# Kernel optimization log

Hardware: AMD Instinct MI355X
Metric: run time of the kernel (lower is better)

## Reference

```python
import jax, jax.numpy as jnp
import numpy as np

B, T, C = 4, 2048, 1024
H, D = 16, 64  # num_heads, head_dim
WINDOW = 256


def setup_inputs() -> dict:
    key = jax.random.key(0)
    k_x, k_qkv, k_proj, k_qb, k_pb = jax.random.split(key, 5)
    x = jax.random.normal(k_x, (B, T, C), dtype=jnp.float32)
    # xavier-uniform-ish init for qkv weight (as in _reset_parameters)
    lim_qkv = float(np.sqrt(6.0 / (C + 3 * C)))
    qkv_w = jax.random.uniform(k_qkv, (3 * C, C), minval=-lim_qkv, maxval=lim_qkv, dtype=jnp.float32)
    qkv_b = jax.random.normal(k_qb, (3 * C,), dtype=jnp.float32) * 0.02
    lim_p = float(np.sqrt(1.0 / C))
    proj_w = jax.random.uniform(k_proj, (C, C), minval=-lim_p, maxval=lim_p, dtype=jnp.float32)
    proj_b = jax.random.normal(k_pb, (C,), dtype=jnp.float32) * 0.02
    # windowed causal mask: attend to j iff j <= i and i - j < WINDOW
    i = jnp.arange(T)[:, None]
    j = jnp.arange(T)[None, :]
    attn_mask = (j <= i) & (i - j < WINDOW)  # [T, T] bool
    return {"x": x, "attn_mask": attn_mask, "qkv_w": qkv_w, "qkv_b": qkv_b,
            "proj_w": proj_w, "proj_b": proj_b}


def reference(x, attn_mask, qkv_w, qkv_b, proj_w, proj_b):
    qkv = (x @ qkv_w.T + qkv_b).reshape(B, T, 3, H, D)
    qkv = jnp.transpose(qkv, (2, 0, 3, 1, 4))
    q, k, v = qkv[0], qkv[1], qkv[2]
    scale = 1.0 / jnp.sqrt(jnp.asarray(D, dtype=q.dtype))
    scores = jnp.einsum('bhqd,bhkd->bhqk', q, k) * scale  # [B,H,T,T]
    neg = jnp.asarray(jnp.finfo(scores.dtype).min, dtype=scores.dtype)
    scores = jnp.where(attn_mask[None, None], scores, neg)
    attn = jax.nn.softmax(scores, axis=-1)
    out = jnp.einsum('bhqk,bhkd->bhqd', attn, v)  # [B,H,T,D]
    out = jnp.transpose(out, (0, 2, 1, 3)).reshape(B, T, C)
    out = out @ proj_w.T + proj_b
    return out
```

## Files before the change

### kernel.cpp

```cpp
#include <hip/hip_runtime.h>

#define BB 4
#define TT 2048
#define CC 1024
#define HH 16
#define DD 64
#define WIN 256

typedef __attribute__((ext_vector_type(8))) short short8;
typedef __attribute__((ext_vector_type(4))) float floatx4;
typedef unsigned short u16;

typedef __attribute__((address_space(3))) void lds_void;
typedef const __attribute__((address_space(1))) void g_void;

__device__ __forceinline__ void gl_lds16(const u16* g, u16* l) {
    __builtin_amdgcn_global_load_lds((g_void*)g, (lds_void*)l, 16, 0, 0);
}

__device__ __forceinline__ float bf2f(u16 u) {
    union { unsigned int i; float f; } v; v.i = ((unsigned int)u) << 16; return v.f;
}
__device__ __forceinline__ u16 f2bf(float f) {
    union { float f; unsigned int i; } v; v.f = f;
    unsigned int x = v.i;
    x += ((x >> 16) & 1u) + 0x7FFFu;
    return (u16)(x >> 16);
}

__global__ void cvt_all(const float* __restrict__ x, const float* __restrict__ qw,
                        const float* __restrict__ pw,
                        u16* __restrict__ xb, u16* __restrict__ wb, u16* __restrict__ pwb) {
    int bid = blockIdx.x;
    const float* src; u16* dst; int off;
    if (bid < 4096)      { src = x;  dst = xb;  off = bid; }
    else if (bid < 5632) { src = qw; dst = wb;  off = bid - 4096; }
    else                 { src = pw; dst = pwb; off = bid - 5632; }
    int i = (off * 256 + (int)threadIdx.x) * 8;
    float4 a = *(const float4*)(src + i);
    float4 b = *(const float4*)(src + i + 4);
    u16 o[8] = { f2bf(a.x), f2bf(a.y), f2bf(a.z), f2bf(a.w),
                 f2bf(b.x), f2bf(b.y), f2bf(b.z), f2bf(b.w) };
    *(uint4*)(dst + i) = *(const uint4*)o;
}


__global__ __launch_bounds__(256) void gemm_qkv(
    const u16* __restrict__ A, const u16* __restrict__ Bw,
    const float* __restrict__ bias,
    u16* __restrict__ Qb, u16* __restrict__ Kb, u16* __restrict__ Vb)
{
    const int K = CC;
    __shared__ u16 As[4096];
    __shared__ u16 Bs[4096];
    const int tid = threadIdx.x;
    const int wave = tid >> 6, lane = tid & 63;
    const int wm = wave >> 1, wn = wave & 1;
    const int quad = lane >> 4, l15 = lane & 15;
    const int bN = blockIdx.x * 128, bM = blockIdx.y * 128;

    const int srow0 = wave * 16 + (lane >> 2);
    const int srow1 = (wave + 4) * 16 + (lane >> 2);
    const int schunk = ((lane & 3) ^ ((lane >> 3) & 3)) * 8;
    const u16* gA0 = A + (size_t)(bM + srow0) * K + schunk;
    const u16* gA1 = A + (size_t)(bM + srow1) * K + schunk;
    const u16* gB0 = Bw + (size_t)(bN + srow0) * K + schunk;
    const u16* gB1 = Bw + (size_t)(bN + srow1) * K + schunk;
    u16* lA0 = &As[wave * 512];
    u16* lA1 = &As[(wave + 4) * 512];
    u16* lB0 = &Bs[wave * 512];
    u16* lB1 = &Bs[(wave + 4) * 512];

    const int rdoff = l15 * 32 + ((quad ^ ((l15 >> 1) & 3)) * 8);

    floatx4 acc[4][4] = {};

    for (int k0 = 0; k0 < K; k0 += 32) {
        __syncthreads();
        gl_lds16(gA0 + k0, lA0);
        gl_lds16(gA1 + k0, lA1);
        gl_lds16(gB0 + k0, lB0);
        gl_lds16(gB1 + k0, lB1);
        __syncthreads();
        short8 af[4], bf[4];
#pragma unroll
        for (int i = 0; i < 4; ++i) {
            af[i] = *(const short8*)&As[(wm * 4 + i) * 512 + rdoff];
            bf[i] = *(const short8*)&Bs[(wn * 4 + i) * 512 + rdoff];
        }
#pragma unroll
        for (int mi = 0; mi < 4; ++mi)
#pragma unroll
            for (int ni = 0; ni < 4; ++ni)
                acc[mi][ni] = __builtin_amdgcn_mfma_f32_16x16x32_bf16(af[mi], bf[ni], acc[mi][ni], 0, 0, 0);
    }

#pragma unroll
    for (int mi = 0; mi < 4; ++mi)
#pragma unroll
        for (int ni = 0; ni < 4; ++ni) {
            int col = bN + wn * 64 + ni * 16 + l15;
            float bv = bias[col];
            int which = col >> 10, rem = col & 1023;
            int h = rem >> 6, d = rem & 63;
            u16* dst = which == 0 ? Qb : (which == 1 ? Kb : Vb);
#pragma unroll
            for (int rg = 0; rg < 4; ++rg) {
                int row = bM + wm * 64 + mi * 16 + quad * 4 + rg;
                int b = row >> 11, t = row & 2047;
                float v = acc[mi][ni][rg] + bv;
                dst[(((size_t)(b * HH + h)) * TT + t) * DD + d] = f2bf(v);
            }
        }
}

__global__ __launch_bounds__(256) void gemm_proj(
    const u16* __restrict__ A, const u16* __restrict__ Bw,
    const float* __restrict__ bias, float* __restrict__ Out)
{
    const int K = CC;
    __shared__ u16 As[4096];
    __shared__ u16 Bs[4096];
    const int tid = threadIdx.x;
    const int wave = tid >> 6, lane = tid & 63;
    const int wm = wave >> 1, wn = wave & 1;
    const int quad = lane >> 4, l15 = lane & 15;
    const int bN = blockIdx.x * 128, bM = blockIdx.y * 128;

    const int srow0 = wave * 16 + (lane >> 2);
    const int srow1 = (wave + 4) * 16 + (lane >> 2);
    const int schunk = ((lane & 3) ^ ((lane >> 3) & 3)) * 8;
    const u16* gA0 = A + (size_t)(bM + srow0) * K + schunk;
    const u16* gA1 = A + (size_t)(bM + srow1) * K + schunk;
    const u16* gB0 = Bw + (size_t)(bN + srow0) * K + schunk;
    const u16* gB1 = Bw + (size_t)(bN + srow1) * K + schunk;
    u16* lA0 = &As[wave * 512];
    u16* lA1 = &As[(wave + 4) * 512];
    u16* lB0 = &Bs[wave * 512];
    u16* lB1 = &Bs[(wave + 4) * 512];

    const int rdoff = l15 * 32 + ((quad ^ ((l15 >> 1) & 3)) * 8);

    floatx4 acc[4][4] = {};

    for (int k0 = 0; k0 < K; k0 += 32) {
        __syncthreads();
        gl_lds16(gA0 + k0, lA0);
        gl_lds16(gA1 + k0, lA1);
        gl_lds16(gB0 + k0, lB0);
        gl_lds16(gB1 + k0, lB1);
        __syncthreads();
        short8 af[4], bf[4];
#pragma unroll
        for (int i = 0; i < 4; ++i) {
            af[i] = *(const short8*)&As[(wm * 4 + i) * 512 + rdoff];
            bf[i] = *(const short8*)&Bs[(wn * 4 + i) * 512 + rdoff];
        }
#pragma unroll
        for (int mi = 0; mi < 4; ++mi)
#pragma unroll
            for (int ni = 0; ni < 4; ++ni)
                acc[mi][ni] = __builtin_amdgcn_mfma_f32_16x16x32_bf16(af[mi], bf[ni], acc[mi][ni], 0, 0, 0);
    }

#pragma unroll
    for (int mi = 0; mi < 4; ++mi)
#pragma unroll
        for (int ni = 0; ni < 4; ++ni) {
            int col = bN + wn * 64 + ni * 16 + l15;
            float bv = bias[col];
#pragma unroll
            for (int rg = 0; rg < 4; ++rg) {
                int row = bM + wm * 64 + mi * 16 + quad * 4 + rg;
                Out[(size_t)row * CC + col] = acc[mi][ni][rg] + bv;
            }
        }
}

__global__ __launch_bounds__(256) void attn_mfma(
    const u16* __restrict__ Qb, const u16* __restrict__ Kb, const u16* __restrict__ Vb,
    u16* __restrict__ Y)
{
    __shared__ u16 Ks[64][72];
    __shared__ u16 Vt[64][72];
    __shared__ u16 Ps[4][16][72];

    const int tid = threadIdx.x;
    const int wave = tid >> 6, lane = tid & 63;
    const int quad = lane >> 4, l15 = lane & 15;
    const int q0 = blockIdx.x * 64;
    const int bh = blockIdx.y;
    const int b = bh >> 4, h = bh & 15;
    const u16* Qp = Qb + (size_t)bh * TT * DD;
    const u16* Kp = Kb + (size_t)bh * TT * DD;
    const u16* Vp = Vb + (size_t)bh * TT * DD;
    const int qw = q0 + wave * 16;

    short8 qf[2];
    qf[0] = *(const short8*)&Qp[(size_t)(qw + l15) * DD + quad * 8];
    qf[1] = *(const short8*)&Qp[(size_t)(qw + l15) * DD + 32 + quad * 8];

    float m_i[4] = { -1e30f, -1e30f, -1e30f, -1e30f };
    float l_i[4] = { 0.f, 0.f, 0.f, 0.f };
    floatx4 Oacc[4] = {};

    const int kb = (q0 >= WIN) ? (q0 - WIN) : 0;
    for (int j0 = kb; j0 < q0 + 64; j0 += 64) {
        __syncthreads();
#pragma unroll
        for (int it = 0; it < 2; ++it) {
            int slot = tid + it * 256;
            int j = slot >> 3, c8 = (slot & 7) << 3;
            *(uint4*)&Ks[j][c8] = *(const uint4*)&Kp[(size_t)(j0 + j) * DD + c8];
        }
#pragma unroll
        for (int it = 0; it < 2; ++it) {
            int slot = tid + it * 256;
            int j = slot >> 3, d0 = (slot & 7) << 3;
            uint4 raw = *(const uint4*)&Vp[(size_t)(j0 + j) * DD + d0];
            const u16* u = (const u16*)&raw;
#pragma unroll
            for (int i = 0; i < 8; ++i) {
                int d = d0 + i;
                int col = (((j >> 3) ^ (d >> 3)) << 3) + (j & 7);
                Vt[d][col] = u[i];
            }
        }
        __syncthreads();

        floatx4 Sacc[4] = {};
#pragma unroll
        for (int nt = 0; nt < 4; ++nt) {
            short8 kf0 = *(const short8*)&Ks[nt * 16 + l15][quad * 8];
            short8 kf1 = *(const short8*)&Ks[nt * 16 + l15][32 + quad * 8];
            Sacc[nt] = __builtin_amdgcn_mfma_f32_16x16x32_bf16(qf[0], kf0, Sacc[nt], 0, 0, 0);
            Sacc[nt] = __builtin_amdgcn_mfma_f32_16x16x32_bf16(qf[1], kf1, Sacc[nt], 0, 0, 0);
        }

        float mc[4] = { -1e30f, -1e30f, -1e30f, -1e30f };
#pragma unroll
        for (int nt = 0; nt < 4; ++nt)
#pragma unroll
            for (int r = 0; r < 4; ++r) {
                int q = qw + quad * 4 + r;
                int j = j0 + nt * 16 + l15;
                float s = (j <= q && (q - j) < WIN) ? Sacc[nt][r] * 0.125f : -1e30f;
                Sacc[nt][r] = s;
                mc[r] = fmaxf(mc[r], s);
            }
#pragma unroll
        for (int m = 1; m < 16; m <<= 1)
#pragma unroll
            for (int r = 0; r < 4; ++r) mc[r] = fmaxf(mc[r], __shfl_xor(mc[r], m, 64));

        float alpha[4];
#pragma unroll
        for (int r = 0; r < 4; ++r) {
            float mn = fmaxf(m_i[r], mc[r]);
            alpha[r] = __expf(m_i[r] - mn);
            m_i[r] = mn;
        }
        float rs[4] = { 0.f, 0.f, 0.f, 0.f };
#pragma unroll
        for (int nt = 0; nt < 4; ++nt)
#pragma unroll
            for (int r = 0; r < 4; ++r) {
                float s = Sacc[nt][r];
                float p = (s > -1e29f) ? __expf(s - m_i[r]) : 0.f;
                Sacc[nt][r] = p;
                rs[r] += p;
            }
#pragma unroll
        for (int m = 1; m < 16; m <<= 1)
#pragma unroll
            for (int r = 0; r < 4; ++r) rs[r] += __shfl_xor(rs[r], m, 64);
#pragma unroll
        for (int r = 0; r < 4; ++r) l_i[r] = l_i[r] * alpha[r] + rs[r];
#pragma unroll
        for (int dt = 0; dt < 4; ++dt)
#pragma unroll
            for (int r = 0; r < 4; ++r) Oacc[dt][r] *= alpha[r];

#pragma unroll
        for (int nt = 0; nt < 4; ++nt)
#pragma unroll
            for (int r = 0; r < 4; ++r)
                Ps[wave][quad * 4 + r][nt * 16 + l15] = f2bf(Sacc[nt][r]);

#pragma unroll
        for (int ks = 0; ks < 2; ++ks) {
            short8 pf = *(const short8*)&Ps[wave][l15][ks * 32 + quad * 8];
#pragma unroll
            for (int dt = 0; dt < 4; ++dt) {
                int d = dt * 16 + l15;
                int col = (((ks * 4 + quad) ^ (d >> 3)) << 3);
                short8 vf = *(const short8*)&Vt[d][col];
                Oacc[dt] = __builtin_amdgcn_mfma_f32_16x16x32_bf16(pf, vf, Oacc[dt], 0, 0, 0);
            }
        }
    }

    float inv[4];
#pragma unroll
    for (int r = 0; r < 4; ++r) inv[r] = 1.f / l_i[r];
#pragma unroll
    for (int dt = 0; dt < 4; ++dt)
#pragma unroll
        for (int r = 0; r < 4; ++r) {
            int t = qw + quad * 4 + r;
            int d = dt * 16 + l15;
            Y[((size_t)b * TT + t) * CC + h * DD + d] = f2bf(Oacc[dt][r] * inv[r]);
        }
}

extern "C" void kernel_launch(void* const* d_in, const int* in_sizes, int n_in,
                              void* d_out, int out_size, void* d_ws, size_t ws_size,
                              hipStream_t stream) {
    const float* x      = (const float*)d_in[0];
    const float* qkv_w  = (const float*)d_in[2];
    const float* qkv_b  = (const float*)d_in[3];
    const float* proj_w = (const float*)d_in[4];
    const float* proj_b = (const float*)d_in[5];
    float* out = (float*)d_out;

    u16* xb  = (u16*)d_ws;
    u16* wb  = xb  + (size_t)8192 * 1024;
    u16* pwb = wb  + (size_t)3072 * 1024;
    u16* Qb  = pwb + (size_t)1024 * 1024;
    u16* Kb  = Qb  + (size_t)64 * 2048 * 64;
    u16* Vb  = Kb  + (size_t)64 * 2048 * 64;
    u16* Yb  = Vb  + (size_t)64 * 2048 * 64;

    cvt_all<<<6144, 256, 0, stream>>>(x, qkv_w, proj_w, xb, wb, pwb);
    gemm_qkv<<<dim3(24, 64), 256, 0, stream>>>(xb, wb, qkv_b, Qb, Kb, Vb);
    attn_mfma<<<dim3(TT / 64, BB * HH), 256, 0, stream>>>(Qb, Kb, Vb, Yb);
    gemm_proj<<<dim3(8, 64), 256, 0, stream>>>(Yb, pwb, proj_b, out);
}
```

Measured before the change: 238.5 us.

## Pipeline QKV GEMM with 256x256 tiles, 8 waves and double-buffered LDS

Rewrites the QKV projection GEMM to use 256x256 block tiles with 512 threads, a double-buffered LDS staging scheme of 64-wide K slices, and interleaved direct-to-LDS global loads with MFMA phases gated by partial vmcnt waits and s_barrier. MFMA sections are raised in priority with s_setprio. The intent is to hide global-load latency behind compute and raise arithmetic intensity per block. In exchange it uses 128KB of LDS per block and more accumulators per wave, which limits occupancy, and the schedule depends on getting the barrier and waitcnt placement right.

After: 245.0 us. 1.03x slower.

```diff
diff --git a/kernel.cpp b/kernel.cpp
--- a/kernel.cpp
+++ b/kernel.cpp
@@ -44,71 +44,109 @@
     *(uint4*)(dst + i) = *(const uint4*)o;
 }
 
-
-__global__ __launch_bounds__(256) void gemm_qkv(
+#define NT_QKV 16
+
+__global__ __launch_bounds__(512, 2) void gemm_qkv(
     const u16* __restrict__ A, const u16* __restrict__ Bw,
     const float* __restrict__ bias,
     u16* __restrict__ Qb, u16* __restrict__ Kb, u16* __restrict__ Vb)
 {
     const int K = CC;
-    __shared__ u16 As[4096];
-    __shared__ u16 Bs[4096];
+    __shared__ u16 lds[2][4][8192];
+
     const int tid = threadIdx.x;
     const int wave = tid >> 6, lane = tid & 63;
-    const int wm = wave >> 1, wn = wave & 1;
+    const int wm = wave >> 2, wn = wave & 3;
     const int quad = lane >> 4, l15 = lane & 15;
-    const int bN = blockIdx.x * 128, bM = blockIdx.y * 128;
-
-    const int srow0 = wave * 16 + (lane >> 2);
-    const int srow1 = (wave + 4) * 16 + (lane >> 2);
-    const int schunk = ((lane & 3) ^ ((lane >> 3) & 3)) * 8;
-    const u16* gA0 = A + (size_t)(bM + srow0) * K + schunk;
-    const u16* gA1 = A + (size_t)(bM + srow1) * K + schunk;
-    const u16* gB0 = Bw + (size_t)(bN + srow0) * K + schunk;
-    const u16* gB1 = Bw + (size_t)(bN + srow1) * K + schunk;
-    u16* lA0 = &As[wave * 512];
-    u16* lA1 = &As[(wave + 4) * 512];
-    u16* lB0 = &Bs[wave * 512];
-    u16* lB1 = &Bs[(wave + 4) * 512];
+    const int bN = blockIdx.x * 256, bM = blockIdx.y * 256;
+
+    const int n0 = tid, n1 = tid + 512;
+    const int r0 = (n0 >> 6) * 16 + ((n0 & 63) >> 2);
+    const int r1 = (n1 >> 6) * 16 + ((n1 & 63) >> 2);
+    const int c0 = (n0 & 3) ^ ((r0 >> 1) & 3);
+    const int c1 = (n1 & 3) ^ ((r1 >> 1) & 3);
+    const u16* gA0 = A + (size_t)(bM + r0) * K + c0 * 8;
+    const u16* gA1 = A + (size_t)(bM + r1) * K + c1 * 8;
+    const u16* gB0 = Bw + (size_t)(bN + r0) * K + c0 * 8;
+    const u16* gB1 = Bw + (size_t)(bN + r1) * K + c1 * 8;
 
     const int rdoff = l15 * 32 + ((quad ^ ((l15 >> 1) & 3)) * 8);
 
-    floatx4 acc[4][4] = {};
-
-    for (int k0 = 0; k0 < K; k0 += 32) {
-        __syncthreads();
-        gl_lds16(gA0 + k0, lA0);
-        gl_lds16(gA1 + k0, lA1);
-        gl_lds16(gB0 + k0, lB0);
-        gl_lds16(gB1 + k0, lB1);
-        __syncthreads();
+    floatx4 acc[8][4] = {};
+
+#define STG_A(buf, kh, t) do { const int ko = (t) * 64 + (kh) * 32;          \
+        gl_lds16(gA0 + ko, &lds[buf][kh][wave * 512]);                       \
+        gl_lds16(gA1 + ko, &lds[buf][kh][4096 + wave * 512]); } while (0)
+#define STG_B(buf, kh, t) do { const int ko = (t) * 64 + (kh) * 32;          \
+        gl_lds16(gB0 + ko, &lds[buf][2 + (kh)][wave * 512]);                 \
+        gl_lds16(gB1 + ko, &lds[buf][2 + (kh)][4096 + wave * 512]); } while (0)
+#define LDA(buf, kk, qm) do { _Pragma("unroll")                              \
+        for (int i = 0; i < 4; ++i)                                          \
+            af[i] = *(const short8*)&lds[buf][kk][(wm * 8 + (qm) * 4 + i) * 512 + rdoff]; } while (0)
+#define LDB(buf, kk) do { _Pragma("unroll")                                  \
+        for (int j = 0; j < 4; ++j)                                          \
+            bf[j] = *(const short8*)&lds[buf][2 + (kk)][(wn * 4 + j) * 512 + rdoff]; } while (0)
+#define MM(qm) do { __builtin_amdgcn_s_setprio(1); _Pragma("unroll")         \
+        for (int i = 0; i < 4; ++i) { _Pragma("unroll")                      \
+            for (int j = 0; j < 4; ++j)                                      \
+                acc[(qm) * 4 + i][j] = __builtin_amdgcn_mfma_f32_16x16x32_bf16( \
+                    af[i], bf[j], acc[(qm) * 4 + i][j], 0, 0, 0); }          \
+        __builtin_amdgcn_s_setprio(0); } while (0)
+#define BARX() do { asm volatile("" ::: "memory");                           \
+        __builtin_amdgcn_s_barrier();                                        \
+        asm volatile("" ::: "memory"); } while (0)
+#define VM6() asm volatile("s_waitcnt vmcnt(6)" ::: "memory")
+
+    STG_B(0, 0, 0); STG_A(0, 0, 0); STG_B(0, 1, 0); STG_A(0, 1, 0);
+    STG_B(1, 0, 1); STG_A(1, 0, 1); STG_B(1, 1, 1);
+    VM6();
+    BARX();
+
+    for (int ii = 0; ii < NT_QKV / 2; ++ii) {
+        const int t0 = 2 * ii, t1 = 2 * ii + 1;
+        const int t2 = (t0 + 2 < NT_QKV) ? t0 + 2 : t0;
+        const int t3 = (t1 + 2 < NT_QKV) ? t1 + 2 : t1;
         short8 af[4], bf[4];
-#pragma unroll
-        for (int i = 0; i < 4; ++i) {
-            af[i] = *(const short8*)&As[(wm * 4 + i) * 512 + rdoff];
-            bf[i] = *(const short8*)&Bs[(wn * 4 + i) * 512 + rdoff];
-        }
-#pragma unroll
-        for (int mi = 0; mi < 4; ++mi)
-#pragma unroll
-            for (int ni = 0; ni < 4; ++ni)
-                acc[mi][ni] = __builtin_amdgcn_mfma_f32_16x16x32_bf16(af[mi], bf[ni], acc[mi][ni], 0, 0, 0);
+        LDA(0, 0, 0); LDB(0, 0); STG_A(1, 1, t1);
+        BARX(); MM(0); BARX();
+        LDA(0, 0, 1); STG_B(0, 0, t2);
+        BARX(); MM(1); BARX();
+        LDA(0, 1, 0); LDB(0, 1); STG_A(0, 0, t2);
+        BARX(); MM(0); BARX();
+        LDA(0, 1, 1); STG_B(0, 1, t2); VM6();
+        BARX(); MM(1); BARX();
+        LDA(1, 0, 0); LDB(1, 0); STG_A(0, 1, t2);
+        BARX(); MM(0); BARX();
+        LDA(1, 0, 1); STG_B(1, 0, t3);
+        BARX(); MM(1); BARX();
+        LDA(1, 1, 0); LDB(1, 1); STG_A(1, 0, t3);
+        BARX(); MM(0); BARX();
+        LDA(1, 1, 1); STG_B(1, 1, t3); VM6();
+        BARX(); MM(1); BARX();
     }
 
-#pragma unroll
-    for (int mi = 0; mi < 4; ++mi)
-#pragma unroll
-        for (int ni = 0; ni < 4; ++ni) {
-            int col = bN + wn * 64 + ni * 16 + l15;
+#undef STG_A
+#undef STG_B
+#undef LDA
+#undef LDB
+#undef MM
+#undef BARX
+#undef VM6
+
+#pragma unroll
+    for (int mf = 0; mf < 8; ++mf)
+#pragma unroll
+        for (int nf = 0; nf < 4; ++nf) {
+            int col = bN + wn * 64 + nf * 16 + l15;
             float bv = bias[col];
             int which = col >> 10, rem = col & 1023;
             int h = rem >> 6, d = rem & 63;
             u16* dst = which == 0 ? Qb : (which == 1 ? Kb : Vb);
 #pragma unroll
             for (int rg = 0; rg < 4; ++rg) {
-                int row = bM + wm * 64 + mi * 16 + quad * 4 + rg;
+                int row = bM + wm * 128 + mf * 16 + quad * 4 + rg;
                 int b = row >> 11, t = row & 2047;
-                float v = acc[mi][ni][rg] + bv;
+                float v = acc[mf][nf][rg] + bv;
                 dst[(((size_t)(b * HH + h)) * TT + t) * DD + d] = f2bf(v);
             }
         }
@@ -332,7 +370,7 @@
     u16* Yb  = Vb  + (size_t)64 * 2048 * 64;
 
     cvt_all<<<6144, 256, 0, stream>>>(x, qkv_w, proj_w, xb, wb, pwb);
-    gemm_qkv<<<dim3(24, 64), 256, 0, stream>>>(xb, wb, qkv_b, Qb, Kb, Vb);
+    gemm_qkv<<<dim3(12, 32), 512, 0, stream>>>(xb, wb, qkv_b, Qb, Kb, Vb);
     attn_mfma<<<dim3(TT / 64, BB * HH), 256, 0, stream>>>(Qb, Kb, Vb, Yb);
     gemm_proj<<<dim3(8, 64), 256, 0, stream>>>(Yb, pwb, proj_b, out);
 }
```

## Pipeline both GEMMs with double-buffered async LDS staging and larger tiles

Applied to the files above, without the earlier changes.

Rewrites the shared QKV and projection GEMM body to use 512-thread blocks with 256x128 output tiles. Global-to-LDS loads are double-buffered at 64-wide K steps, and partial vmcnt waits let the next K slice load while MFMAs run. Block IDs are swizzled so neighbouring blocks reuse the same tiles in L2, and s_setprio raises priority around the MFMA bursts. The larger LDS footprint (about 96KB per block) limits residency to one block per CU, and the last iterations issue redundant clamped loads.

After: 263.2 us. 10.4% more time.

```diff
diff --git a/kernel.cpp b/kernel.cpp
--- a/kernel.cpp
+++ b/kernel.cpp
@@ -45,137 +45,118 @@
 }
 
 
-__global__ __launch_bounds__(256) void gemm_qkv(
-    const u16* __restrict__ A, const u16* __restrict__ Bw,
+#define STG(buf, kh, t) do { const int ko = (t) * 64 + (kh) * 32;            \
+        gl_lds16(gA0 + ko, &lA[buf][kh][wave * 512]);                        \
+        gl_lds16(gA1 + ko, &lA[buf][kh][4096 + wave * 512]);                 \
+        gl_lds16(gB0 + ko, &lB[buf][kh][wave * 512]); } while (0)
+#define LDAB(buf, kk) do { _Pragma("unroll")                                 \
+        for (int i = 0; i < 4; ++i)                                          \
+            af[i] = *(const short8*)&lA[buf][kk][(wm * 4 + i) * 512 + rdoff];\
+        _Pragma("unroll")                                                    \
+        for (int j = 0; j < 4; ++j)                                          \
+            bf[j] = *(const short8*)&lB[buf][kk][(wn * 4 + j) * 512 + rdoff]; } while (0)
+#define MM() do { __builtin_amdgcn_s_setprio(1); _Pragma("unroll")           \
+        for (int i = 0; i < 4; ++i) { _Pragma("unroll")                      \
+            for (int j = 0; j < 4; ++j)                                      \
+                acc[i][j] = __builtin_amdgcn_mfma_f32_16x16x32_bf16(         \
+                    af[i], bf[j], acc[i][j], 0, 0, 0); }                     \
+        __builtin_amdgcn_s_setprio(0); } while (0)
+#define BARX() do { asm volatile("" ::: "memory");                           \
+        __builtin_amdgcn_s_barrier();                                        \
+        asm volatile("" ::: "memory"); } while (0)
+#define VM6() asm volatile("s_waitcnt vmcnt(6)" ::: "memory")
+
+#define GEMM_BODY                                                            \
+    const int K = CC;                                                        \
+    __shared__ u16 lA[2][2][8192];                                           \
+    __shared__ u16 lB[2][2][4096];                                           \
+    const int tid = threadIdx.x;                                             \
+    const int wave = tid >> 6, lane = tid & 63;                              \
+    const int wm = wave >> 1, wn = wave & 1;                                 \
+    const int quad = lane >> 4, l15 = lane & 15;                             \
+    const int r0 = wave * 16 + (lane >> 2);                                  \
+    const int r1 = r0 + 128;                                                 \
+    const int c0 = (lane & 3) ^ ((r0 >> 1) & 3);                             \
+    const u16* gA0 = Amat + (size_t)(bM + r0) * K + c0 * 8;                  \
+    const u16* gA1 = Amat + (size_t)(bM + r1) * K + c0 * 8;                  \
+    const u16* gB0 = Bw + (size_t)(bN + r0) * K + c0 * 8;                    \
+    const int rdoff = l15 * 32 + ((quad ^ ((l15 >> 1) & 3)) * 8);            \
+    floatx4 acc[4][4] = {};                                                  \
+    STG(0, 0, 0); STG(0, 1, 0); STG(1, 0, 1);                                \
+    VM6(); BARX();                                                           \
+    for (int ii = 0; ii < 8; ++ii) {                                         \
+        const int t0 = 2 * ii, t1 = t0 + 1;                                  \
+        const int t2 = (t0 + 2 < 16) ? t0 + 2 : t0;                          \
+        const int t3 = (t1 + 2 < 16) ? t1 + 2 : t1;                          \
+        short8 af[4], bf[4];                                                 \
+        LDAB(0, 0); STG(1, 1, t1); VM6(); BARX(); MM(); BARX();              \
+        LDAB(0, 1); STG(0, 0, t2); VM6(); BARX(); MM(); BARX();              \
+        LDAB(1, 0); STG(0, 1, t2); VM6(); BARX(); MM(); BARX();              \
+        LDAB(1, 1); STG(1, 0, t3); VM6(); BARX(); MM(); BARX();              \
+    }
+
+__global__ __launch_bounds__(512, 2) void gemm_qkv(
+    const u16* __restrict__ Amat, const u16* __restrict__ Bw,
     const float* __restrict__ bias,
     u16* __restrict__ Qb, u16* __restrict__ Kb, u16* __restrict__ Vb)
 {
-    const int K = CC;
-    __shared__ u16 As[4096];
-    __shared__ u16 Bs[4096];
-    const int tid = threadIdx.x;
-    const int wave = tid >> 6, lane = tid & 63;
-    const int wm = wave >> 1, wn = wave & 1;
-    const int quad = lane >> 4, l15 = lane & 15;
-    const int bN = blockIdx.x * 128, bM = blockIdx.y * 128;
-
-    const int srow0 = wave * 16 + (lane >> 2);
-    const int srow1 = (wave + 4) * 16 + (lane >> 2);
-    const int schunk = ((lane & 3) ^ ((lane >> 3) & 3)) * 8;
-    const u16* gA0 = A + (size_t)(bM + srow0) * K + schunk;
-    const u16* gA1 = A + (size_t)(bM + srow1) * K + schunk;
-    const u16* gB0 = Bw + (size_t)(bN + srow0) * K + schunk;
-    const u16* gB1 = Bw + (size_t)(bN + srow1) * K + schunk;
-    u16* lA0 = &As[wave * 512];
-    u16* lA1 = &As[(wave + 4) * 512];
-    u16* lB0 = &Bs[wave * 512];
-    u16* lB1 = &Bs[(wave + 4) * 512];
-
-    const int rdoff = l15 * 32 + ((quad ^ ((l15 >> 1) & 3)) * 8);
-
-    floatx4 acc[4][4] = {};
-
-    for (int k0 = 0; k0 < K; k0 += 32) {
-        __syncthreads();
-        gl_lds16(gA0 + k0, lA0);
-        gl_lds16(gA1 + k0, lA1);
-        gl_lds16(gB0 + k0, lB0);
-        gl_lds16(gB1 + k0, lB1);
-        __syncthreads();
-        short8 af[4], bf[4];
-#pragma unroll
-        for (int i = 0; i < 4; ++i) {
-            af[i] = *(const short8*)&As[(wm * 4 + i) * 512 + rdoff];
-            bf[i] = *(const short8*)&Bs[(wn * 4 + i) * 512 + rdoff];
-        }
-#pragma unroll
-        for (int mi = 0; mi < 4; ++mi)
-#pragma unroll
-            for (int ni = 0; ni < 4; ++ni)
-                acc[mi][ni] = __builtin_amdgcn_mfma_f32_16x16x32_bf16(af[mi], bf[ni], acc[mi][ni], 0, 0, 0);
-    }
-
-#pragma unroll
-    for (int mi = 0; mi < 4; ++mi)
-#pragma unroll
-        for (int ni = 0; ni < 4; ++ni) {
-            int col = bN + wn * 64 + ni * 16 + l15;
+    const int raw = blockIdx.x;
+    const int swz = (raw & 7) * 96 + (raw >> 3);
+    const int bN = (swz >> 5) * 128;
+    const int bM = (swz & 31) * 256;
+
+    GEMM_BODY
+
+#pragma unroll
+    for (int mf = 0; mf < 4; ++mf)
+#pragma unroll
+        for (int nf = 0; nf < 4; ++nf) {
+            int col = bN + wn * 64 + nf * 16 + l15;
             float bv = bias[col];
             int which = col >> 10, rem = col & 1023;
             int h = rem >> 6, d = rem & 63;
             u16* dst = which == 0 ? Qb : (which == 1 ? Kb : Vb);
 #pragma unroll
             for (int rg = 0; rg < 4; ++rg) {
-                int row = bM + wm * 64 + mi * 16 + quad * 4 + rg;
+                int row = bM + wm * 64 + mf * 16 + quad * 4 + rg;
                 int b = row >> 11, t = row & 2047;
-                float v = acc[mi][ni][rg] + bv;
+                float v = acc[mf][nf][rg] + bv;
                 dst[(((size_t)(b * HH + h)) * TT + t) * DD + d] = f2bf(v);
             }
         }
 }
 
-__global__ __launch_bounds__(256) void gemm_proj(
-    const u16* __restrict__ A, const u16* __restrict__ Bw,
+__global__ __launch_bounds__(512, 2) void gemm_proj(
+    const u16* __restrict__ Amat, const u16* __restrict__ Bw,
     const float* __restrict__ bias, float* __restrict__ Out)
 {
-    const int K = CC;
-    __shared__ u16 As[4096];
-    __shared__ u16 Bs[4096];
-    const int tid = threadIdx.x;
-    const int wave = tid >> 6, lane = tid & 63;
-    const int wm = wave >> 1, wn = wave & 1;
-    const int quad = lane >> 4, l15 = lane & 15;
-    const int bN = blockIdx.x * 128, bM = blockIdx.y * 128;
-
-    const int srow0 = wave * 16 + (lane >> 2);
-    const int srow1 = (wave + 4) * 16 + (lane >> 2);
-    const int schunk = ((lane & 3) ^ ((lane >> 3) & 3)) * 8;
-    const u16* gA0 = A + (size_t)(bM + srow0) * K + schunk;
-    const u16* gA1 = A + (size_t)(bM + srow1) * K + schunk;
-    const u16* gB0 = Bw + (size_t)(bN + srow0) * K + schunk;
-    const u16* gB1 = Bw + (size_t)(bN + srow1) * K + schunk;
-    u16* lA0 = &As[wave * 512];
-    u16* lA1 = &As[(wave + 4) * 512];
-    u16* lB0 = &Bs[wave * 512];
-    u16* lB1 = &Bs[(wave + 4) * 512];
-
-    const int rdoff = l15 * 32 + ((quad ^ ((l15 >> 1) & 3)) * 8);
-
-    floatx4 acc[4][4] = {};
-
-    for (int k0 = 0; k0 < K; k0 += 32) {
-        __syncthreads();
-        gl_lds16(gA0 + k0, lA0);
-        gl_lds16(gA1 + k0, lA1);
-        gl_lds16(gB0 + k0, lB0);
-        gl_lds16(gB1 + k0, lB1);
-        __syncthreads();
-        short8 af[4], bf[4];
-#pragma unroll
-        for (int i = 0; i < 4; ++i) {
-            af[i] = *(const short8*)&As[(wm * 4 + i) * 512 + rdoff];
-            bf[i] = *(const short8*)&Bs[(wn * 4 + i) * 512 + rdoff];
-        }
-#pragma unroll
-        for (int mi = 0; mi < 4; ++mi)
-#pragma unroll
-            for (int ni = 0; ni < 4; ++ni)
-                acc[mi][ni] = __builtin_amdgcn_mfma_f32_16x16x32_bf16(af[mi], bf[ni], acc[mi][ni], 0, 0, 0);
-    }
-
-#pragma unroll
-    for (int mi = 0; mi < 4; ++mi)
-#pragma unroll
-        for (int ni = 0; ni < 4; ++ni) {
-            int col = bN + wn * 64 + ni * 16 + l15;
+    const int raw = blockIdx.x;
+    const int swz = (raw & 7) * 32 + (raw >> 3);
+    const int bN = (swz >> 5) * 128;
+    const int bM = (swz & 31) * 256;
+
+    GEMM_BODY
+
+#pragma unroll
+    for (int mf = 0; mf < 4; ++mf)
+#pragma unroll
+        for (int nf = 0; nf < 4; ++nf) {
+            int col = bN + wn * 64 + nf * 16 + l15;
             float bv = bias[col];
 #pragma unroll
             for (int rg = 0; rg < 4; ++rg) {
-                int row = bM + wm * 64 + mi * 16 + quad * 4 + rg;
-                Out[(size_t)row * CC + col] = acc[mi][ni][rg] + bv;
-            }
-        }
-}
+                int row = bM + wm * 64 + mf * 16 + quad * 4 + rg;
+                Out[(size_t)row * CC + col] = acc[mf][nf][rg] + bv;
+            }
+        }
+}
+
+#undef STG
+#undef LDAB
+#undef MM
+#undef BARX
+#undef VM6
+#undef GEMM_BODY
 
 __global__ __launch_bounds__(256) void attn_mfma(
     const u16* __restrict__ Qb, const u16* __restrict__ Kb, const u16* __restrict__ Vb,
@@ -332,7 +313,7 @@
     u16* Yb  = Vb  + (size_t)64 * 2048 * 64;
 
     cvt_all<<<6144, 256, 0, stream>>>(x, qkv_w, proj_w, xb, wb, pwb);
-    gemm_qkv<<<dim3(24, 64), 256, 0, stream>>>(xb, wb, qkv_b, Qb, Kb, Vb);
+    gemm_qkv<<<768, 512, 0, stream>>>(xb, wb, qkv_b, Qb, Kb, Vb);
     attn_mfma<<<dim3(TT / 64, BB * HH), 256, 0, stream>>>(Qb, Kb, Vb, Yb);
-    gemm_proj<<<dim3(8, 64), 256, 0, stream>>>(Yb, pwb, proj_b, out);
-}
+    gemm_proj<<<256, 512, 0, stream>>>(Yb, pwb, proj_b, out);
+}
```
